# Optimization experiments

Measured on AMD Instinct MI355X. Metric: run time of the kernel, lower is better.

## Reference

```python
import jax, jax.numpy as jnp
import numpy as np

N_NODES = 50000
N_EDGES = 1600000
IN_CH = 128
HID = 64
HEADS = 2
EMB = 128
OUT_CH = EMB // HEADS  # 64, GATConvMean out_channels
NEG_SLOPE = 0.2


def _gat_conv(x, src, dst, W, a_src, a_dst, b, heads, out_ch, concat, n_nodes):
    # x: [N, F_in]; W: [F_in, heads*out_ch]; a_src/a_dst: [heads, out_ch]; b: bias
    s = (x @ W).reshape(n_nodes, heads, out_ch)          # [N, H, C]
    alpha_src = jnp.sum(s * a_src, axis=-1)              # [N, H]
    alpha_dst = jnp.sum(s * a_dst, axis=-1)              # [N, H]
    e = jax.nn.leaky_relu(alpha_src[src] + alpha_dst[dst], NEG_SLOPE)  # [E, H]
    # segment softmax over edges sharing the same destination node
    m = jax.ops.segment_max(e, dst, num_segments=n_nodes)             # [N, H]
    ex = jnp.exp(e - m[dst])
    denom = jax.ops.segment_sum(ex, dst, num_segments=n_nodes)        # [N, H]
    alpha = ex / denom[dst]                                           # [E, H]
    msg = s[src] * alpha[:, :, None]                                  # [E, H, C]
    out = jax.ops.segment_sum(msg, dst, num_segments=n_nodes)         # [N, H, C]
    if concat:
        out = out.reshape(n_nodes, heads * out_ch)
    else:
        out = out.mean(axis=1)
    return out + b


def setup_inputs() -> dict:
    key = jax.random.key(0)
    ks = jax.random.split(key, 16)
    X = jax.random.normal(ks[0], (N_NODES, IN_CH), dtype=jnp.float32)
    edge_index = jax.random.randint(ks[1], (2, N_EDGES), 0, N_NODES, dtype=jnp.int64)

    def glorot(k, shape):
        fan_in, fan_out = shape[0], shape[-1]
        lim = jnp.sqrt(6.0 / (fan_in + fan_out)).astype(jnp.float32)
        return jax.random.uniform(k, shape, jnp.float32, -lim, lim)

    HC = HEADS * HID  # 128
    # in_layer: GATConv(IN_CH -> HID, heads=HEADS, concat)
    W0 = glorot(ks[2], (IN_CH, HC))
    a_src0 = glorot(ks[3], (HEADS, HID))
    a_dst0 = glorot(ks[4], (HEADS, HID))
    b0 = jnp.zeros((HC,), jnp.float32)
    # middle layer: GATConv(HC -> HID, heads=HEADS, concat)
    W1 = glorot(ks[5], (HC, HC))
    a_src1 = glorot(ks[6], (HEADS, HID))
    a_dst1 = glorot(ks[7], (HEADS, HID))
    b1 = jnp.zeros((HC,), jnp.float32)
    # ivectors: GATConvMean(HC -> OUT_CH, heads=HEADS, mean over heads)
    W2 = glorot(ks[8], (HC, HEADS * OUT_CH))
    a_src2 = glorot(ks[9], (HEADS, OUT_CH))
    a_dst2 = glorot(ks[10], (HEADS, OUT_CH))
    b2 = jnp.zeros((OUT_CH,), jnp.float32)
    return {
        "X": X, "edge_index": edge_index,
        "W0": W0, "a_src0": a_src0, "a_dst0": a_dst0, "b0": b0,
        "W1": W1, "a_src1": a_src1, "a_dst1": a_dst1, "b1": b1,
        "W2": W2, "a_src2": a_src2, "a_dst2": a_dst2, "b2": b2,
    }


def reference(X, edge_index, W0, a_src0, a_dst0, b0, W1, a_src1, a_dst1, b1, W2, a_src2, a_dst2, b2):
    n = X.shape[0]
    loop = jnp.arange(n, dtype=edge_index.dtype)
    src = jnp.concatenate([edge_index[0], loop])  # PyG GATConv add_self_loops=True
    dst = jnp.concatenate([edge_index[1], loop])
    h = jax.nn.elu(_gat_conv(X, src, dst, W0, a_src0, a_dst0, b0, HEADS, HID, True, n))
    h = jax.nn.relu(_gat_conv(h, src, dst, W1, a_src1, a_dst1, b1, HEADS, HID, True, n))
    # dropout is identity in eval mode
    out = jax.nn.relu(_gat_conv(h, src, dst, W2, a_src2, a_dst2, b2, HEADS, OUT_CH, False, n))
    return out
```

## Files before the change

### kernel.cpp

```cpp
#include <hip/hip_runtime.h>
#include <hip/hip_bf16.h>


#define SCAN_BLOCK 256

__global__ void detect_i64(const unsigned* __restrict__ ei, int* __restrict__ flag) {
    if (threadIdx.x == 0 && blockIdx.x == 0) {
        int allz = 1;
        for (int i = 0; i < 128; ++i)
            if (ei[2 * i + 1] != 0u) { allz = 0; break; }
        *flag = allz;
    }
}

__global__ __launch_bounds__(256) void gat_rank(
    const void* __restrict__ ei, const int* __restrict__ flag, int nE, int nN,
    int* __restrict__ cnt, int* __restrict__ rank,
    int* __restrict__ srci, int* __restrict__ dsti) {
    const int i64 = *flag;
    const long long total = (long long)nE + nN;
    const long long stride = (long long)gridDim.x * blockDim.x;
    for (long long i = (long long)blockIdx.x * blockDim.x + threadIdx.x; i < total; i += stride) {
        int s, d;
        if (i < nE) {
            if (i64) { s = (int)((const long long*)ei)[i]; d = (int)((const long long*)ei)[nE + i]; }
            else     { s = ((const int*)ei)[i];            d = ((const int*)ei)[nE + i]; }
        } else { s = d = (int)(i - nE); }
        srci[i] = s;
        dsti[i] = d;
        rank[i] = atomicAdd(&cnt[d], 1);
    }
}

__global__ __launch_bounds__(SCAN_BLOCK) void scan_stage1(
    const int* __restrict__ cnt, int* __restrict__ partial, int* __restrict__ bsum, int n) {
    __shared__ int tmp[SCAN_BLOCK];
    const int i = blockIdx.x * SCAN_BLOCK + threadIdx.x;
    const int v = (i < n) ? cnt[i] : 0;
    tmp[threadIdx.x] = v;
    __syncthreads();
    #pragma unroll
    for (int off = 1; off < SCAN_BLOCK; off <<= 1) {
        const int t = (threadIdx.x >= off) ? tmp[threadIdx.x - off] : 0;
        __syncthreads();
        tmp[threadIdx.x] += t;
        __syncthreads();
    }
    if (i < n) partial[i] = tmp[threadIdx.x];
    if (threadIdx.x == SCAN_BLOCK - 1) bsum[blockIdx.x] = tmp[threadIdx.x];
}

__global__ void scan_stage2(int* __restrict__ bsum, int nb, int* __restrict__ rowp, int n) {
    const int lane = threadIdx.x;
    int carry = 0;
    for (int base = 0; base < nb; base += 64) {
        const int i = base + lane;
        const int v = (i < nb) ? bsum[i] : 0;
        int incl = v;
        #pragma unroll
        for (int off = 1; off < 64; off <<= 1) {
            const int t = __shfl_up(incl, off);
            if (lane >= off) incl += t;
        }
        if (i < nb) bsum[i] = carry + incl - v;
        carry += __shfl(incl, 63);
    }
    if (lane == 0) rowp[n] = carry;
}

__global__ __launch_bounds__(SCAN_BLOCK) void scan_stage3(
    const int* __restrict__ partial, const int* __restrict__ cnt, const int* __restrict__ bsum,
    int* __restrict__ rowp, int n) {
    const int i = blockIdx.x * SCAN_BLOCK + threadIdx.x;
    if (i < n) rowp[i] = bsum[i >> 8] + partial[i] - cnt[i];
}

__global__ __launch_bounds__(256) void gat_place(
    const int* __restrict__ srci, const int* __restrict__ dsti,
    const int* __restrict__ rank, const int* __restrict__ rowp,
    long long total, int nN, int* __restrict__ csr) {
    const int cw = (nN + 7) >> 3;
    const int lo = (blockIdx.x & 7) * cw;
    const long long stride = (long long)(gridDim.x >> 3) * blockDim.x;
    for (long long i = (long long)(blockIdx.x >> 3) * blockDim.x + threadIdx.x;
         i < total; i += stride) {
        const int d = dsti[i];
        if ((unsigned)(d - lo) >= (unsigned)cw) continue;
        csr[rowp[d] + rank[i]] = srci[i];
    }
}

__global__ __launch_bounds__(256) void gemm_alpha(
    const float* __restrict__ Xin, const float* __restrict__ W,
    const float* __restrict__ avs, const float* __restrict__ avd,
    float* __restrict__ S, float* __restrict__ as_, float* __restrict__ ad_, int n) {
    __shared__ float Xl[64][128];
    const int tid = threadIdx.x;
    const int row0 = blockIdx.x * 64;
    for (int i = tid; i < 64 * 32; i += 256) {
        const int r = i >> 5, c4 = i & 31;
        const int gr = row0 + r;
        float4 v = (gr < n) ? ((const float4*)(Xin + (size_t)gr * 128))[c4]
                            : make_float4(0.f, 0.f, 0.f, 0.f);
        ((float4*)(&Xl[r][0]))[c4] = v;
    }
    __syncthreads();
    const int col4 = tid & 31;
    const int rowg = tid >> 5;
    float4 acc[8];
    #pragma unroll
    for (int r = 0; r < 8; ++r) acc[r] = make_float4(0.f, 0.f, 0.f, 0.f);
    const float* Wc = W + col4 * 4;
    for (int kk = 0; kk < 128; kk += 4) {
        const float4 w0 = *(const float4*)(Wc + (size_t)(kk + 0) * 128);
        const float4 w1 = *(const float4*)(Wc + (size_t)(kk + 1) * 128);
        const float4 w2 = *(const float4*)(Wc + (size_t)(kk + 2) * 128);
        const float4 w3 = *(const float4*)(Wc + (size_t)(kk + 3) * 128);
        #pragma unroll
        for (int r = 0; r < 8; ++r) {
            const float4 x = *(const float4*)(&Xl[rowg * 8 + r][kk]);
            acc[r].x = fmaf(x.x, w0.x, acc[r].x); acc[r].y = fmaf(x.x, w0.y, acc[r].y);
            acc[r].z = fmaf(x.x, w0.z, acc[r].z); acc[r].w = fmaf(x.x, w0.w, acc[r].w);
            acc[r].x = fmaf(x.y, w1.x, acc[r].x); acc[r].y = fmaf(x.y, w1.y, acc[r].y);
            acc[r].z = fmaf(x.y, w1.z, acc[r].z); acc[r].w = fmaf(x.y, w1.w, acc[r].w);
            acc[r].x = fmaf(x.z, w2.x, acc[r].x); acc[r].y = fmaf(x.z, w2.y, acc[r].y);
            acc[r].z = fmaf(x.z, w2.z, acc[r].z); acc[r].w = fmaf(x.z, w2.w, acc[r].w);
            acc[r].x = fmaf(x.w, w3.x, acc[r].x); acc[r].y = fmaf(x.w, w3.y, acc[r].y);
            acc[r].z = fmaf(x.w, w3.z, acc[r].z); acc[r].w = fmaf(x.w, w3.w, acc[r].w);
        }
    }
    const float4 av = ((const float4*)avs)[col4];
    const float4 dv = ((const float4*)avd)[col4];
    #pragma unroll
    for (int r = 0; r < 8; ++r) {
        const int grow = row0 + rowg * 8 + r;
        if (grow < n) ((float4*)(S + (size_t)grow * 128))[col4] = acc[r];
        float ps = acc[r].x * av.x + acc[r].y * av.y + acc[r].z * av.z + acc[r].w * av.w;
        float pd = acc[r].x * dv.x + acc[r].y * dv.y + acc[r].z * dv.z + acc[r].w * dv.w;
        #pragma unroll
        for (int off = 8; off; off >>= 1) {
            ps += __shfl_xor(ps, off);
            pd += __shfl_xor(pd, off);
        }
        if ((col4 & 15) == 0 && grow < n) {
            const int h = col4 >> 4;
            as_[2 * grow + h] = ps;
            ad_[2 * grow + h] = pd;
        }
    }
}

__global__ __launch_bounds__(256) void gat_fused(
    const float* __restrict__ S, const float* __restrict__ as_,
    const float* __restrict__ ad_, const int* __restrict__ rowp,
    const int* __restrict__ csr, const float* __restrict__ bias,
    float* __restrict__ out, int n, int mode) {
    const int lane = threadIdx.x & 63;
    const int d = (blockIdx.x * blockDim.x + threadIdx.x) >> 6;
    if (d >= n) return;
    const int beg = rowp[d], end = rowp[d + 1];
    const int deg = end - beg;
    const float2 adv = *(const float2*)(ad_ + 2 * d);
    const int g = lane >> 4;
    const int gl = lane & 15;
    float4 acc0 = make_float4(0.f, 0.f, 0.f, 0.f);
    float4 acc1 = make_float4(0.f, 0.f, 0.f, 0.f);
    if (deg <= 64) {
        const bool has = lane < deg;
        const int s_reg = has ? csr[beg + lane] : 0;
        float e0 = -1e30f, e1 = -1e30f;
        if (has) {
            const float2 asv = *(const float2*)(as_ + 2 * s_reg);
            e0 = asv.x + adv.x; e0 = e0 > 0.f ? e0 : 0.2f * e0;
            e1 = asv.y + adv.y; e1 = e1 > 0.f ? e1 : 0.2f * e1;
        }
        float m0 = e0, m1 = e1;
        #pragma unroll
        for (int off = 32; off; off >>= 1) {
            m0 = fmaxf(m0, __shfl_xor(m0, off));
            m1 = fmaxf(m1, __shfl_xor(m1, off));
        }
        const float p0 = has ? __expf(e0 - m0) : 0.f;
        const float p1 = has ? __expf(e1 - m1) : 0.f;
        float s0 = p0, s1 = p1;
        #pragma unroll
        for (int off = 32; off; off >>= 1) {
            s0 += __shfl_xor(s0, off);
            s1 += __shfl_xor(s1, off);
        }
        const float inv0 = 1.f / s0, inv1 = 1.f / s1;
        int k = 0;
        for (; k + 4 <= deg; k += 4) {
            const int ke = k + g;
            const int sv = __shfl(s_reg, ke);
            const float a0 = __shfl(p0, ke) * inv0;
            const float a1 = __shfl(p1, ke) * inv1;
            const float4* r = (const float4*)(S + ((size_t)sv << 7));
            const float4 v0 = r[gl], v1 = r[16 + gl];
            acc0.x = fmaf(a0, v0.x, acc0.x); acc0.y = fmaf(a0, v0.y, acc0.y);
            acc0.z = fmaf(a0, v0.z, acc0.z); acc0.w = fmaf(a0, v0.w, acc0.w);
            acc1.x = fmaf(a1, v1.x, acc1.x); acc1.y = fmaf(a1, v1.y, acc1.y);
            acc1.z = fmaf(a1, v1.z, acc1.z); acc1.w = fmaf(a1, v1.w, acc1.w);
        }
        if (k < deg) {
            const int ke = k + g;
            const bool valid = ke < deg;
            const int idx = valid ? ke : 0;
            const int sv = __shfl(s_reg, idx);
            const float q0 = __shfl(p0, idx), q1 = __shfl(p1, idx);
            const float a0 = valid ? q0 * inv0 : 0.f;
            const float a1 = valid ? q1 * inv1 : 0.f;
            const float4* r = (const float4*)(S + ((size_t)sv << 7));
            const float4 v0 = r[gl], v1 = r[16 + gl];
            acc0.x = fmaf(a0, v0.x, acc0.x); acc0.y = fmaf(a0, v0.y, acc0.y);
            acc0.z = fmaf(a0, v0.z, acc0.z); acc0.w = fmaf(a0, v0.w, acc0.w);
            acc1.x = fmaf(a1, v1.x, acc1.x); acc1.y = fmaf(a1, v1.y, acc1.y);
            acc1.z = fmaf(a1, v1.z, acc1.z); acc1.w = fmaf(a1, v1.w, acc1.w);
        }
    } else {
        float m0 = -1e30f, m1 = -1e30f;
        for (int i = beg + lane; i < end; i += 64) {
            const int s = csr[i];
            const float2 asv = *(const float2*)(as_ + 2 * s);
            float e0 = asv.x + adv.x; e0 = e0 > 0.f ? e0 : 0.2f * e0;
            float e1 = asv.y + adv.y; e1 = e1 > 0.f ? e1 : 0.2f * e1;
            m0 = fmaxf(m0, e0); m1 = fmaxf(m1, e1);
        }
        #pragma unroll
        for (int off = 32; off; off >>= 1) {
            m0 = fmaxf(m0, __shfl_xor(m0, off));
            m1 = fmaxf(m1, __shfl_xor(m1, off));
        }
        float s0 = 0.f, s1 = 0.f;
        for (int i = beg + lane; i < end; i += 64) {
            const int s = csr[i];
            const float2 asv = *(const float2*)(as_ + 2 * s);
            float e0 = asv.x + adv.x; e0 = e0 > 0.f ? e0 : 0.2f * e0;
            float e1 = asv.y + adv.y; e1 = e1 > 0.f ? e1 : 0.2f * e1;
            s0 += __expf(e0 - m0); s1 += __expf(e1 - m1);
        }
        #pragma unroll
        for (int off = 32; off; off >>= 1) {
            s0 += __shfl_xor(s0, off);
            s1 += __shfl_xor(s1, off);
        }
        const float inv0 = 1.f / s0, inv1 = 1.f / s1;
        for (int k = 0; k < deg; k += 4) {
            const int ke = k + g;
            const bool valid = ke < deg;
            const int j = beg + (valid ? ke : 0);
            const int sv = csr[j];
            const float2 asv = *(const float2*)(as_ + 2 * sv);
            float e0 = asv.x + adv.x; e0 = e0 > 0.f ? e0 : 0.2f * e0;
            float e1 = asv.y + adv.y; e1 = e1 > 0.f ? e1 : 0.2f * e1;
            const float a0 = valid ? __expf(e0 - m0) * inv0 : 0.f;
            const float a1 = valid ? __expf(e1 - m1) * inv1 : 0.f;
            const float4* r = (const float4*)(S + ((size_t)sv << 7));
            const float4 v0 = r[gl], v1 = r[16 + gl];
            acc0.x = fmaf(a0, v0.x, acc0.x); acc0.y = fmaf(a0, v0.y, acc0.y);
            acc0.z = fmaf(a0, v0.z, acc0.z); acc0.w = fmaf(a0, v0.w, acc0.w);
            acc1.x = fmaf(a1, v1.x, acc1.x); acc1.y = fmaf(a1, v1.y, acc1.y);
            acc1.z = fmaf(a1, v1.z, acc1.z); acc1.w = fmaf(a1, v1.w, acc1.w);
        }
    }
    #pragma unroll
    for (int off = 16; off <= 32; off <<= 1) {
        acc0.x += __shfl_xor(acc0.x, off); acc0.y += __shfl_xor(acc0.y, off);
        acc0.z += __shfl_xor(acc0.z, off); acc0.w += __shfl_xor(acc0.w, off);
        acc1.x += __shfl_xor(acc1.x, off); acc1.y += __shfl_xor(acc1.y, off);
        acc1.z += __shfl_xor(acc1.z, off); acc1.w += __shfl_xor(acc1.w, off);
    }
    if (mode == 2) {
        if (lane < 16) {
            const float4 b = ((const float4*)bias)[gl];
            float4 o;
            o.x = fmaxf(0.5f * (acc0.x + acc1.x) + b.x, 0.f);
            o.y = fmaxf(0.5f * (acc0.y + acc1.y) + b.y, 0.f);
            o.z = fmaxf(0.5f * (acc0.z + acc1.z) + b.z, 0.f);
            o.w = fmaxf(0.5f * (acc0.w + acc1.w) + b.w, 0.f);
            ((float4*)(out + (size_t)d * 64))[gl] = o;
        }
    } else if (lane < 32) {
        const int ci = (lane < 16) ? gl : 16 + gl;
        const float4 a = (lane < 16) ? acc0 : acc1;
        const float4 b = ((const float4*)bias)[ci];
        float4 o;
        o.x = a.x + b.x; o.y = a.y + b.y; o.z = a.z + b.z; o.w = a.w + b.w;
        if (mode == 0) {
            o.x = o.x > 0.f ? o.x : expm1f(o.x);
            o.y = o.y > 0.f ? o.y : expm1f(o.y);
            o.z = o.z > 0.f ? o.z : expm1f(o.z);
            o.w = o.w > 0.f ? o.w : expm1f(o.w);
        } else {
            o.x = fmaxf(o.x, 0.f); o.y = fmaxf(o.y, 0.f);
            o.z = fmaxf(o.z, 0.f); o.w = fmaxf(o.w, 0.f);
        }
        ((float4*)(out + (size_t)d * 128))[ci] = o;
    }
}

extern "C" void kernel_launch(void* const* d_in, const int* in_sizes, int n_in,
                              void* d_out, int out_size, void* d_ws, size_t ws_size,
                              hipStream_t stream) {
    const float* X   = (const float*)d_in[0];
    const void*  EI  = d_in[1];
    const float* W0  = (const float*)d_in[2];
    const float* as0 = (const float*)d_in[3];
    const float* ad0 = (const float*)d_in[4];
    const float* b0  = (const float*)d_in[5];
    const float* W1  = (const float*)d_in[6];
    const float* as1 = (const float*)d_in[7];
    const float* ad1 = (const float*)d_in[8];
    const float* b1  = (const float*)d_in[9];
    const float* W2  = (const float*)d_in[10];
    const float* as2 = (const float*)d_in[11];
    const float* ad2 = (const float*)d_in[12];
    const float* b2  = (const float*)d_in[13];

    const int N  = in_sizes[0] / 128;
    const int E  = in_sizes[1] / 2;
    const int ET = E + N;
    const int NB = (N + SCAN_BLOCK - 1) / SCAN_BLOCK;

    char* p = (char*)d_ws;
    size_t used = 0;
    auto alloc = [&](size_t bytes) -> void* {
        void* r = p + used;
        used += (bytes + 255) & ~(size_t)255;
        return r;
    };
    float*  S    = (float*)alloc((size_t)N * 128 * 4);
    float*  H0   = (float*)alloc((size_t)N * 128 * 4);
    float*  H1   = (float*)alloc((size_t)N * 128 * 4);
    int*    csr  = (int*)alloc((size_t)ET * 4);
    int*    rowp = (int*)alloc((size_t)(N + 1) * 4);
    int*    cnt  = (int*)alloc((size_t)N * 4);
    int*    part = (int*)alloc((size_t)N * 4);
    int*    bsum = (int*)alloc((size_t)NB * 4);
    float*  asb  = (float*)alloc((size_t)N * 2 * 4);
    float*  adb  = (float*)alloc((size_t)N * 2 * 4);
    int*    flag = (int*)alloc(256);
    if (used > ws_size) return;
    const int ETP = (ET + 63) & ~63;
    int* srci = (int*)S;
    int* dsti = srci + ETP;
    int* rank = dsti + ETP;

    hipMemsetAsync(cnt, 0, (size_t)N * 4, stream);
    detect_i64<<<1, 64, 0, stream>>>((const unsigned*)EI, flag);
    gat_rank<<<2048, 256, 0, stream>>>(EI, flag, E, N, cnt, rank, srci, dsti);
    scan_stage1<<<NB, SCAN_BLOCK, 0, stream>>>(cnt, part, bsum, N);
    scan_stage2<<<1, 64, 0, stream>>>(bsum, NB, rowp, N);
    scan_stage3<<<NB, SCAN_BLOCK, 0, stream>>>(part, cnt, bsum, rowp, N);
    gat_place<<<2048, 256, 0, stream>>>(srci, dsti, rank, rowp, (long long)ET, N, csr);

    const int gemm_blocks = (N + 63) / 64;
    const int wave_blocks = (N + 3) / 4;

    gemm_alpha<<<gemm_blocks, 256, 0, stream>>>(X, W0, as0, ad0, S, asb, adb, N);
    gat_fused<<<wave_blocks, 256, 0, stream>>>(S, asb, adb, rowp, csr, b0, H0, N, 0);
    gemm_alpha<<<gemm_blocks, 256, 0, stream>>>(H0, W1, as1, ad1, S, asb, adb, N);
    gat_fused<<<wave_blocks, 256, 0, stream>>>(S, asb, adb, rowp, csr, b1, H1, N, 1);
    gemm_alpha<<<gemm_blocks, 256, 0, stream>>>(H1, W2, as2, ad2, S, asb, adb, N);
    gat_fused<<<wave_blocks, 256, 0, stream>>>(S, asb, adb, rowp, csr, b2, (float*)d_out, N, 2);
}
```

Before: 579.8 us.

## Build CSR with partitioned count and atomic cursor scatter instead of ranks

The fused rank-with-atomics pass is split into a plain index conversion and a count kernel that partitions destinations into eight ranges, so atomics from a block stay within one range. The scatter now takes positions from an atomic cursor array initialised from the row pointers, so the per-edge rank array is no longer written or read. This trades rank-array traffic and global atomic spread for an extra pass over dsti and atomics in the scatter. Neighbour order within each row becomes nondeterministic, which can change floating-point summation order.

```diff
diff --git a/kernel.cpp b/kernel.cpp
--- a/kernel.cpp
+++ b/kernel.cpp
@@ -13,9 +13,8 @@
     }
 }
 
-__global__ __launch_bounds__(256) void gat_rank(
+__global__ __launch_bounds__(256) void gat_convert(
     const void* __restrict__ ei, const int* __restrict__ flag, int nE, int nN,
-    int* __restrict__ cnt, int* __restrict__ rank,
     int* __restrict__ srci, int* __restrict__ dsti) {
     const int i64 = *flag;
     const long long total = (long long)nE + nN;
@@ -28,7 +27,19 @@
         } else { s = d = (int)(i - nE); }
         srci[i] = s;
         dsti[i] = d;
-        rank[i] = atomicAdd(&cnt[d], 1);
+    }
+}
+
+__global__ __launch_bounds__(256) void gat_count(
+    const int* __restrict__ dsti, long long total, int nN, int* __restrict__ cnt) {
+    const int cw = (nN + 7) >> 3;
+    const int lo = (blockIdx.x & 7) * cw;
+    const long long stride = (long long)(gridDim.x >> 3) * blockDim.x;
+    for (long long i = (long long)(blockIdx.x >> 3) * blockDim.x + threadIdx.x;
+         i < total; i += stride) {
+        const int d = dsti[i];
+        if ((unsigned)(d - lo) >= (unsigned)cw) continue;
+        atomicAdd(&cnt[d], 1);
     }
 }
 
@@ -70,15 +81,18 @@
 
 __global__ __launch_bounds__(SCAN_BLOCK) void scan_stage3(
     const int* __restrict__ partial, const int* __restrict__ cnt, const int* __restrict__ bsum,
-    int* __restrict__ rowp, int n) {
+    int* __restrict__ rowp, int* __restrict__ cur, int n) {
     const int i = blockIdx.x * SCAN_BLOCK + threadIdx.x;
-    if (i < n) rowp[i] = bsum[i >> 8] + partial[i] - cnt[i];
-}
-
-__global__ __launch_bounds__(256) void gat_place(
+    if (i < n) {
+        const int e = bsum[i >> 8] + partial[i] - cnt[i];
+        rowp[i] = e;
+        cur[i] = e;
+    }
+}
+
+__global__ __launch_bounds__(256) void gat_scatter(
     const int* __restrict__ srci, const int* __restrict__ dsti,
-    const int* __restrict__ rank, const int* __restrict__ rowp,
-    long long total, int nN, int* __restrict__ csr) {
+    long long total, int nN, int* __restrict__ cur, int* __restrict__ csr) {
     const int cw = (nN + 7) >> 3;
     const int lo = (blockIdx.x & 7) * cw;
     const long long stride = (long long)(gridDim.x >> 3) * blockDim.x;
@@ -86,7 +100,8 @@
          i < total; i += stride) {
         const int d = dsti[i];
         if ((unsigned)(d - lo) >= (unsigned)cw) continue;
-        csr[rowp[d] + rank[i]] = srci[i];
+        const int pos = atomicAdd(&cur[d], 1);
+        csr[pos] = srci[i];
     }
 }
 
@@ -335,6 +350,7 @@
     int*    csr  = (int*)alloc((size_t)ET * 4);
     int*    rowp = (int*)alloc((size_t)(N + 1) * 4);
     int*    cnt  = (int*)alloc((size_t)N * 4);
+    int*    cur  = (int*)alloc((size_t)N * 4);
     int*    part = (int*)alloc((size_t)N * 4);
     int*    bsum = (int*)alloc((size_t)NB * 4);
     float*  asb  = (float*)alloc((size_t)N * 2 * 4);
@@ -344,15 +360,15 @@
     const int ETP = (ET + 63) & ~63;
     int* srci = (int*)S;
     int* dsti = srci + ETP;
-    int* rank = dsti + ETP;
 
     hipMemsetAsync(cnt, 0, (size_t)N * 4, stream);
     detect_i64<<<1, 64, 0, stream>>>((const unsigned*)EI, flag);
-    gat_rank<<<2048, 256, 0, stream>>>(EI, flag, E, N, cnt, rank, srci, dsti);
+    gat_convert<<<2048, 256, 0, stream>>>(EI, flag, E, N, srci, dsti);
+    gat_count<<<2048, 256, 0, stream>>>(dsti, (long long)ET, N, cnt);
     scan_stage1<<<NB, SCAN_BLOCK, 0, stream>>>(cnt, part, bsum, N);
     scan_stage2<<<1, 64, 0, stream>>>(bsum, NB, rowp, N);
-    scan_stage3<<<NB, SCAN_BLOCK, 0, stream>>>(part, cnt, bsum, rowp, N);
-    gat_place<<<2048, 256, 0, stream>>>(srci, dsti, rank, rowp, (long long)ET, N, csr);
+    scan_stage3<<<NB, SCAN_BLOCK, 0, stream>>>(part, cnt, bsum, rowp, cur, N);
+    gat_scatter<<<2048, 256, 0, stream>>>(srci, dsti, (long long)ET, N, cur, csr);
 
     const int gemm_blocks = (N + 63) / 64;
     const int wave_blocks = (N + 3) / 4;
```

Result: slower. 596.8 us (+2.9%).
